# Kernel tuning notes

Measured on AMD Instinct MI355X. Metric: run time of the kernel, lower is better.

## Reference

```python
import jax, jax.numpy as jnp
import numpy as np

EMBED_DIM = 1024
LATEN_DIM = 1024
B, S = 4, 2048


def setup_inputs() -> dict:
    key = jax.random.key(0)
    k1, k2, k3, k4, k5 = jax.random.split(key, 5)
    xq = jax.random.normal(k1, (B, S, EMBED_DIM), dtype=jnp.float32)
    xk = jax.random.normal(k2, (B, S, EMBED_DIM), dtype=jnp.float32)
    xv = jax.random.normal(k3, (B, S, EMBED_DIM), dtype=jnp.float32)
    # Linear weight init similar to torch default scale
    bound = 1.0 / np.sqrt(EMBED_DIM)
    Wq = jax.random.uniform(k4, (EMBED_DIM, EMBED_DIM), minval=-bound, maxval=bound, dtype=jnp.float32)
    bq = jax.random.uniform(k5, (EMBED_DIM,), minval=-bound, maxval=bound, dtype=jnp.float32)
    # causal mask: 1 => masked (future positions)
    att_mask = jnp.triu(jnp.ones((S, S), dtype=jnp.int32), k=1)
    return {"xq": xq, "xk": xk, "xv": xv, "Wq": Wq, "bq": bq, "att_mask": att_mask}


def reference(xq, xk, xv, Wq, bq, att_mask):
    scale = LATEN_DIM ** (-0.5)
    # Faithful to source: linearQ is applied to all three inputs.
    Q = jnp.einsum('bsd,ed->bse', xq, Wq) + bq
    K = jnp.einsum('bsd,ed->bse', xk, Wq) + bq
    V = jnp.einsum('bsd,ed->bse', xv, Wq) + bq
    scores = jnp.einsum('bqe,bke->bqk', Q, K) * scale  # [B, S, S]
    scores = jnp.where(att_mask == 1, -jnp.inf, scores)
    probs = jax.nn.softmax(scores, axis=-1)
    return jnp.einsum('bqk,bke->bqe', probs, V)
```

## Files before the change

### kernel.cpp

```cpp
#include <hip/hip_runtime.h>
#include <hip/hip_bf16.h>
#include <stdint.h>


typedef __attribute__((ext_vector_type(8))) short bf16x8;
typedef __attribute__((ext_vector_type(4))) float floatx4;

#define DEVI static __device__ __forceinline__

static constexpr int S_ = 2048;
static constexpr int E_ = 1024;
static constexpr int BATCH = 4;

DEVI unsigned short f2b(float f) {
  union { float f; unsigned u; } v; v.f = f;
  return (unsigned short)((v.u + 0x7FFFu + ((v.u >> 16) & 1u)) >> 16);
}

DEVI void async_load16(const void* g, void* l) {
  __builtin_amdgcn_global_load_lds(
      (__attribute__((address_space(1))) void*)(void*)(g),
      (__attribute__((address_space(3))) void*)(l),
      16, 0, 0);
}

DEVI void mfma_tile(const unsigned short* lsA, const unsigned short* lsB,
                    int m0, int n0, int lrow, int lk, floatx4 (&acc)[4][4]) {
  bf16x8 af[4], bfr[4];
#pragma unroll
  for (int i = 0; i < 4; ++i)
    af[i] = *(const bf16x8*)(lsA + (m0 + i * 16 + lrow) * 32 + lk);
#pragma unroll
  for (int i = 0; i < 4; ++i)
    bfr[i] = *(const bf16x8*)(lsB + (n0 + i * 16 + lrow) * 32 + lk);
#pragma unroll
  for (int mi = 0; mi < 4; ++mi)
#pragma unroll
    for (int ni = 0; ni < 4; ++ni)
      acc[mi][ni] = __builtin_amdgcn_mfma_f32_16x16x32_bf16(
          af[mi], bfr[ni], acc[mi][ni], 0, 0, 0);
}

DEVI void stage_bf16(const unsigned short* src, unsigned short* ls, int ld,
                     int tid) {
#pragma unroll
  for (int j = 0; j < 2; ++j) {
    int t = tid + j * 256, row = t >> 2, kk = (t & 3) << 3;
    async_load16(src + (size_t)row * ld + kk, ls + t * 8);
  }
}

__global__ void cvt_kernel(const float* __restrict__ src,
                           unsigned short* __restrict__ dst, int n4) {
  int i = blockIdx.x * blockDim.x + threadIdx.x;
  if (i < n4) {
    float4 v = ((const float4*)src)[i];
    ushort4 o;
    o.x = f2b(v.x); o.y = f2b(v.y); o.z = f2b(v.z); o.w = f2b(v.w);
    ((ushort4*)dst)[i] = o;
  }
}

__global__ __launch_bounds__(256, 2) void gemm_qkv(
    const float* __restrict__ xq, const float* __restrict__ xk,
    const float* __restrict__ xv, const unsigned short* __restrict__ Wb,
    const float* __restrict__ bias, unsigned short* __restrict__ Qb,
    unsigned short* __restrict__ Kb, unsigned short* __restrict__ Vt) {
  __shared__ __align__(16) unsigned short lsA[128 * 32];
  __shared__ __align__(16) unsigned short lsB[128 * 32];
  const int l = blockIdx.x;
  const int xcd = l & 7, i = l >> 3;
  const int bn = i & 7;
  const int bmg = xcd * 24 + (i >> 3);
  const int input = bmg / 64, bm = bmg % 64;
  const float* A = (input == 0) ? xq : (input == 1) ? xk : xv;
  A += (size_t)bm * 128 * 1024;

  const int tid = threadIdx.x;
  const int lane = tid & 63, wave = tid >> 6;
  const int m0 = (wave >> 1) * 64, n0 = (wave & 1) * 64;
  const int lrow = lane & 15, lk = (lane >> 4) * 8;

  floatx4 acc[4][4] = {};

  for (int kt = 0; kt < 1024 / 32; ++kt) {
    if (kt) __syncthreads();
    stage_bf16(Wb + (size_t)bn * 128 * 1024 + kt * 32, lsB, 1024, tid);
#pragma unroll
    for (int j = 0; j < 4; ++j) {
      int t = tid + j * 256, row = t >> 3, kk = (t & 7) << 2;
      float4 v = *(const float4*)(A + (size_t)row * 1024 + kt * 32 + kk);
      ushort4 o;
      o.x = f2b(v.x); o.y = f2b(v.y); o.z = f2b(v.z); o.w = f2b(v.w);
      *(ushort4*)(lsA + row * 32 + kk) = o;
    }
    __syncthreads();
    mfma_tile(lsA, lsB, m0, n0, lrow, lk, acc);
  }

  unsigned short* C = (input == 0) ? Qb : (input == 1) ? Kb : Vt;
  const int rb = (lane >> 4) * 4;
#pragma unroll
  for (int mi = 0; mi < 4; ++mi)
#pragma unroll
    for (int ni = 0; ni < 4; ++ni) {
      int gcol = bn * 128 + n0 + ni * 16 + lrow;
      float bv = bias[gcol];
#pragma unroll
      for (int r = 0; r < 4; ++r) {
        int grow = bm * 128 + m0 + mi * 16 + rb + r;
        unsigned short val = f2b(acc[mi][ni][r] + bv);
        if (input == 2) {
          int b = grow >> 11, s = grow & 2047;
          C[((size_t)b * 1024 + gcol) * 2048 + s] = val;
        } else {
          C[(size_t)grow * 1024 + gcol] = val;
        }
      }
    }
}

__global__ __launch_bounds__(256, 2) void gemm_scores(
    const unsigned short* __restrict__ Qb,
    const unsigned short* __restrict__ Kb, float* __restrict__ Sc) {
  const int l = blockIdx.x;
  const int xcd = l & 7, k = l >> 3;
  const int m = k & 7, gl = k >> 3;
  const int gg = xcd * 12 + gl;
  const int z = gg / 24, r = gg % 24;
  const int bm = (r < 8) ? r : 8 + ((r - 8) >> 1);
  const int bn = ((r < 8) ? 0 : ((r - 8) & 1)) * 8 + m;
  if (bn > bm) return;

  __shared__ __align__(16) unsigned short lsA[128 * 32];
  __shared__ __align__(16) unsigned short lsB[128 * 32];
  const unsigned short* A = Qb + ((size_t)z * S_ + bm * 128) * E_;
  const unsigned short* Bt = Kb + ((size_t)z * S_ + bn * 128) * E_;
  float* C = Sc + (size_t)z * S_ * S_;
  const int tid = threadIdx.x;
  const int lane = tid & 63, wave = tid >> 6;
  const int m0 = (wave >> 1) * 64, n0 = (wave & 1) * 64;
  const int lrow = lane & 15, lk = (lane >> 4) * 8;

  floatx4 acc[4][4] = {};
  for (int kt = 0; kt < 32; ++kt) {
    if (kt) __syncthreads();
    stage_bf16(A + kt * 32, lsA, E_, tid);
    stage_bf16(Bt + kt * 32, lsB, E_, tid);
    __syncthreads();
    mfma_tile(lsA, lsB, m0, n0, lrow, lk, acc);
  }

  const int rb = (lane >> 4) * 4;
#pragma unroll
  for (int mi = 0; mi < 4; ++mi)
#pragma unroll
    for (int ni = 0; ni < 4; ++ni) {
      int gcol = bn * 128 + n0 + ni * 16 + lrow;
#pragma unroll
      for (int r = 0; r < 4; ++r) {
        int grow = bm * 128 + m0 + mi * 16 + rb + r;
        C[(size_t)grow * S_ + gcol] = acc[mi][ni][r] * 0.03125f;
      }
    }
}

__global__ __launch_bounds__(256, 2) void gemm_pv(
    const unsigned short* __restrict__ Pb,
    const unsigned short* __restrict__ Vt, float* __restrict__ Out) {
  __shared__ __align__(16) unsigned short lsA[128 * 32];
  __shared__ __align__(16) unsigned short lsB[128 * 32];
  const int l = blockIdx.x;
  const int xcd = l & 7, i = l >> 3;
  const int bn = i & 7;
  const int bmg = xcd * 8 + (i >> 3);
  const int z = bmg >> 4, bm = bmg & 15;

  const unsigned short* A = Pb + ((size_t)z * S_ + bm * 128) * (2 * S_);
  const unsigned short* Bt = Vt + ((size_t)z * E_ + bn * 128) * S_;
  float* C = Out + (size_t)z * S_ * E_;
  const int tid = threadIdx.x;
  const int lane = tid & 63, wave = tid >> 6;
  const int m0 = (wave >> 1) * 64, n0 = (wave & 1) * 64;
  const int lrow = lane & 15, lk = (lane >> 4) * 8;

  floatx4 acc[4][4] = {};
  const int nK = (bm + 1) * 4;
  for (int kt = 0; kt < nK; ++kt) {
    if (kt) __syncthreads();
    stage_bf16(A + kt * 32, lsA, 2 * S_, tid);
    stage_bf16(Bt + kt * 32, lsB, S_, tid);
    __syncthreads();
    mfma_tile(lsA, lsB, m0, n0, lrow, lk, acc);
  }

  const int rb = (lane >> 4) * 4;
#pragma unroll
  for (int mi = 0; mi < 4; ++mi)
#pragma unroll
    for (int ni = 0; ni < 4; ++ni) {
      int gcol = bn * 128 + n0 + ni * 16 + lrow;
#pragma unroll
      for (int r = 0; r < 4; ++r) {
        int grow = bm * 128 + m0 + mi * 16 + rb + r;
        C[(size_t)grow * E_ + gcol] = acc[mi][ni][r];
      }
    }
}

__global__ __launch_bounds__(256) void softmax_rows(float* __restrict__ Sc) {
  const int r = blockIdx.x;
  const int q = r & (S_ - 1);
  float* srow = Sc + (size_t)r * S_;
  __shared__ float buf[S_];
  __shared__ float red[8];
  const int tid = threadIdx.x, lane = tid & 63, wv = tid >> 6;
  const int n = q + 1;

  float mx = -1e30f;
  for (int k = tid; k < n; k += 256) {
    float v = srow[k];
    buf[k] = v;
    mx = fmaxf(mx, v);
  }
#pragma unroll
  for (int off = 32; off; off >>= 1) mx = fmaxf(mx, __shfl_xor(mx, off));
  if (lane == 0) red[wv] = mx;
  __syncthreads();
  mx = fmaxf(fmaxf(red[0], red[1]), fmaxf(red[2], red[3]));

  float sum = 0.f;
  for (int k = tid; k < n; k += 256) {
    float e = __expf(buf[k] - mx);
    buf[k] = e;
    sum += e;
  }
#pragma unroll
  for (int off = 32; off; off >>= 1) sum += __shfl_xor(sum, off);
  if (lane == 0) red[4 + wv] = sum;
  __syncthreads();
  sum = red[4] + red[5] + red[6] + red[7];
  const float inv = 1.0f / sum;

  unsigned short* prow = (unsigned short*)srow;
  const int kmax = (q & ~127) + 128;
  for (int k = tid; k < kmax; k += 256)
    prow[k] = (k < n) ? f2b(buf[k] * inv) : (unsigned short)0;
}

extern "C" void kernel_launch(void* const* d_in, const int* in_sizes, int n_in,
                              void* d_out, int out_size, void* d_ws,
                              size_t ws_size, hipStream_t stream) {
  (void)in_sizes; (void)n_in; (void)out_size; (void)ws_size;
  const float* xq = (const float*)d_in[0];
  const float* xk = (const float*)d_in[1];
  const float* xv = (const float*)d_in[2];
  const float* Wq = (const float*)d_in[3];
  const float* bq = (const float*)d_in[4];
  float* out = (float*)d_out;

  unsigned short* Wb = (unsigned short*)d_ws;
  unsigned short* Qb = Wb + (size_t)1024 * 1024;
  unsigned short* Kb = Qb + (size_t)8192 * 1024;
  unsigned short* Vt = Kb + (size_t)8192 * 1024;
  float* Sc = (float*)(Vt + (size_t)8192 * 1024);

  cvt_kernel<<<(1024 * 1024 / 4) / 256, 256, 0, stream>>>(Wq, Wb,
                                                          1024 * 1024 / 4);
  gemm_qkv<<<1536, 256, 0, stream>>>(xq, xk, xv, Wb, bq, Qb, Kb, Vt);
  gemm_scores<<<768, 256, 0, stream>>>(Qb, Kb, Sc);
  softmax_rows<<<BATCH * S_, 256, 0, stream>>>(Sc);
  gemm_pv<<<512, 256, 0, stream>>>((const unsigned short*)Sc, Vt, out);
}
```

Before: 341.0 us.

## Double-buffer LDS tiles in the QKV, scores and PV GEMM kernels

Measured after the change: 344.1 us. Within noise of the previous version (+0.9%).

```diff
diff --git a/kernel.cpp b/kernel.cpp
--- a/kernel.cpp
+++ b/kernel.cpp
@@ -66,8 +66,8 @@
     const float* __restrict__ xv, const unsigned short* __restrict__ Wb,
     const float* __restrict__ bias, unsigned short* __restrict__ Qb,
     unsigned short* __restrict__ Kb, unsigned short* __restrict__ Vt) {
-  __shared__ __align__(16) unsigned short lsA[128 * 32];
-  __shared__ __align__(16) unsigned short lsB[128 * 32];
+  __shared__ __align__(16) unsigned short lsA[2][128 * 32];
+  __shared__ __align__(16) unsigned short lsB[2][128 * 32];
   const int l = blockIdx.x;
   const int xcd = l & 7, i = l >> 3;
   const int bn = i & 7;
@@ -80,22 +80,46 @@
   const int lane = tid & 63, wave = tid >> 6;
   const int m0 = (wave >> 1) * 64, n0 = (wave & 1) * 64;
   const int lrow = lane & 15, lk = (lane >> 4) * 8;
+  const int ar0 = tid >> 3, ak0 = (tid & 7) << 2;
 
   floatx4 acc[4][4] = {};
 
-  for (int kt = 0; kt < 1024 / 32; ++kt) {
-    if (kt) __syncthreads();
-    stage_bf16(Wb + (size_t)bn * 128 * 1024 + kt * 32, lsB, 1024, tid);
+  stage_bf16(Wb + (size_t)bn * 128 * 1024, lsB[0], 1024, tid);
+  {
+    float4 v[4];
+#pragma unroll
+    for (int j = 0; j < 4; ++j)
+      v[j] = *(const float4*)(A + (size_t)(ar0 + j * 32) * 1024 + ak0);
 #pragma unroll
     for (int j = 0; j < 4; ++j) {
-      int t = tid + j * 256, row = t >> 3, kk = (t & 7) << 2;
-      float4 v = *(const float4*)(A + (size_t)row * 1024 + kt * 32 + kk);
       ushort4 o;
-      o.x = f2b(v.x); o.y = f2b(v.y); o.z = f2b(v.z); o.w = f2b(v.w);
-      *(ushort4*)(lsA + row * 32 + kk) = o;
-    }
+      o.x = f2b(v[j].x); o.y = f2b(v[j].y); o.z = f2b(v[j].z); o.w = f2b(v[j].w);
+      *(ushort4*)(lsA[0] + (ar0 + j * 32) * 32 + ak0) = o;
+    }
+  }
+
+  for (int kt = 0; kt < 32; ++kt) {
     __syncthreads();
-    mfma_tile(lsA, lsB, m0, n0, lrow, lk, acc);
+    const int cur = kt & 1, nxt = cur ^ 1;
+    float4 v[4];
+    if (kt < 31) {
+      stage_bf16(Wb + (size_t)bn * 128 * 1024 + (kt + 1) * 32, lsB[nxt], 1024,
+                 tid);
+#pragma unroll
+      for (int j = 0; j < 4; ++j)
+        v[j] = *(const float4*)(A + (size_t)(ar0 + j * 32) * 1024 +
+                                (kt + 1) * 32 + ak0);
+    }
+    mfma_tile(lsA[cur], lsB[cur], m0, n0, lrow, lk, acc);
+    if (kt < 31) {
+#pragma unroll
+      for (int j = 0; j < 4; ++j) {
+        ushort4 o;
+        o.x = f2b(v[j].x); o.y = f2b(v[j].y);
+        o.z = f2b(v[j].z); o.w = f2b(v[j].w);
+        *(ushort4*)(lsA[nxt] + (ar0 + j * 32) * 32 + ak0) = o;
+      }
+    }
   }
 
   unsigned short* C = (input == 0) ? Qb : (input == 1) ? Kb : Vt;
@@ -132,8 +156,8 @@
   const int bn = ((r < 8) ? 0 : ((r - 8) & 1)) * 8 + m;
   if (bn > bm) return;
 
-  __shared__ __align__(16) unsigned short lsA[128 * 32];
-  __shared__ __align__(16) unsigned short lsB[128 * 32];
+  __shared__ __align__(16) unsigned short lsA[2][128 * 32];
+  __shared__ __align__(16) unsigned short lsB[2][128 * 32];
   const unsigned short* A = Qb + ((size_t)z * S_ + bm * 128) * E_;
   const unsigned short* Bt = Kb + ((size_t)z * S_ + bn * 128) * E_;
   float* C = Sc + (size_t)z * S_ * S_;
@@ -143,12 +167,16 @@
   const int lrow = lane & 15, lk = (lane >> 4) * 8;
 
   floatx4 acc[4][4] = {};
+  stage_bf16(A, lsA[0], E_, tid);
+  stage_bf16(Bt, lsB[0], E_, tid);
   for (int kt = 0; kt < 32; ++kt) {
-    if (kt) __syncthreads();
-    stage_bf16(A + kt * 32, lsA, E_, tid);
-    stage_bf16(Bt + kt * 32, lsB, E_, tid);
     __syncthreads();
-    mfma_tile(lsA, lsB, m0, n0, lrow, lk, acc);
+    const int cur = kt & 1, nxt = cur ^ 1;
+    if (kt < 31) {
+      stage_bf16(A + (kt + 1) * 32, lsA[nxt], E_, tid);
+      stage_bf16(Bt + (kt + 1) * 32, lsB[nxt], E_, tid);
+    }
+    mfma_tile(lsA[cur], lsB[cur], m0, n0, lrow, lk, acc);
   }
 
   const int rb = (lane >> 4) * 4;
@@ -168,8 +196,8 @@
 __global__ __launch_bounds__(256, 2) void gemm_pv(
     const unsigned short* __restrict__ Pb,
     const unsigned short* __restrict__ Vt, float* __restrict__ Out) {
-  __shared__ __align__(16) unsigned short lsA[128 * 32];
-  __shared__ __align__(16) unsigned short lsB[128 * 32];
+  __shared__ __align__(16) unsigned short lsA[2][128 * 32];
+  __shared__ __align__(16) unsigned short lsB[2][128 * 32];
   const int l = blockIdx.x;
   const int xcd = l & 7, i = l >> 3;
   const int bn = i & 7;
@@ -186,12 +214,16 @@
 
   floatx4 acc[4][4] = {};
   const int nK = (bm + 1) * 4;
+  stage_bf16(A, lsA[0], 2 * S_, tid);
+  stage_bf16(Bt, lsB[0], S_, tid);
   for (int kt = 0; kt < nK; ++kt) {
-    if (kt) __syncthreads();
-    stage_bf16(A + kt * 32, lsA, 2 * S_, tid);
-    stage_bf16(Bt + kt * 32, lsB, S_, tid);
     __syncthreads();
-    mfma_tile(lsA, lsB, m0, n0, lrow, lk, acc);
+    const int cur = kt & 1, nxt = cur ^ 1;
+    if (kt < nK - 1) {
+      stage_bf16(A + (kt + 1) * 32, lsA[nxt], 2 * S_, tid);
+      stage_bf16(Bt + (kt + 1) * 32, lsB[nxt], S_, tid);
+    }
+    mfma_tile(lsA[cur], lsB[cur], m0, n0, lrow, lk, acc);
   }
 
   const int rb = (lane >> 4) * 4;
```

## Pre-convert activations to bf16 and double the K-step per barrier in GEMMs

Applied to the files above, without the earlier changes.

Measured after the change: 326.2 us. 1.05x faster.

```diff
diff --git a/kernel.cpp b/kernel.cpp
--- a/kernel.cpp
+++ b/kernel.cpp
@@ -61,20 +61,19 @@
   }
 }
 
-__global__ __launch_bounds__(256, 2) void gemm_qkv(
-    const float* __restrict__ xq, const float* __restrict__ xk,
-    const float* __restrict__ xv, const unsigned short* __restrict__ Wb,
+__global__ __launch_bounds__(256) void gemm_qkv(
+    const unsigned short* __restrict__ Xb, const unsigned short* __restrict__ Wb,
     const float* __restrict__ bias, unsigned short* __restrict__ Qb,
     unsigned short* __restrict__ Kb, unsigned short* __restrict__ Vt) {
-  __shared__ __align__(16) unsigned short lsA[128 * 32];
-  __shared__ __align__(16) unsigned short lsB[128 * 32];
+  __shared__ __align__(16) unsigned short lsA[2][128 * 32];
+  __shared__ __align__(16) unsigned short lsB[2][128 * 32];
   const int l = blockIdx.x;
   const int xcd = l & 7, i = l >> 3;
   const int bn = i & 7;
   const int bmg = xcd * 24 + (i >> 3);
   const int input = bmg / 64, bm = bmg % 64;
-  const float* A = (input == 0) ? xq : (input == 1) ? xk : xv;
-  A += (size_t)bm * 128 * 1024;
+  const unsigned short* A = Xb + (size_t)bmg * 128 * 1024;
+  const unsigned short* W = Wb + (size_t)bn * 128 * 1024;
 
   const int tid = threadIdx.x;
   const int lane = tid & 63, wave = tid >> 6;
@@ -83,19 +82,15 @@
 
   floatx4 acc[4][4] = {};
 
-  for (int kt = 0; kt < 1024 / 32; ++kt) {
+  for (int kt = 0; kt < 16; ++kt) {
     if (kt) __syncthreads();
-    stage_bf16(Wb + (size_t)bn * 128 * 1024 + kt * 32, lsB, 1024, tid);
-#pragma unroll
-    for (int j = 0; j < 4; ++j) {
-      int t = tid + j * 256, row = t >> 3, kk = (t & 7) << 2;
-      float4 v = *(const float4*)(A + (size_t)row * 1024 + kt * 32 + kk);
-      ushort4 o;
-      o.x = f2b(v.x); o.y = f2b(v.y); o.z = f2b(v.z); o.w = f2b(v.w);
-      *(ushort4*)(lsA + row * 32 + kk) = o;
-    }
+    stage_bf16(A + kt * 64, lsA[0], 1024, tid);
+    stage_bf16(A + kt * 64 + 32, lsA[1], 1024, tid);
+    stage_bf16(W + kt * 64, lsB[0], 1024, tid);
+    stage_bf16(W + kt * 64 + 32, lsB[1], 1024, tid);
     __syncthreads();
-    mfma_tile(lsA, lsB, m0, n0, lrow, lk, acc);
+    mfma_tile(lsA[0], lsB[0], m0, n0, lrow, lk, acc);
+    mfma_tile(lsA[1], lsB[1], m0, n0, lrow, lk, acc);
   }
 
   unsigned short* C = (input == 0) ? Qb : (input == 1) ? Kb : Vt;
@@ -120,7 +115,7 @@
     }
 }
 
-__global__ __launch_bounds__(256, 2) void gemm_scores(
+__global__ __launch_bounds__(256) void gemm_scores(
     const unsigned short* __restrict__ Qb,
     const unsigned short* __restrict__ Kb, float* __restrict__ Sc) {
   const int l = blockIdx.x;
@@ -132,8 +127,8 @@
   const int bn = ((r < 8) ? 0 : ((r - 8) & 1)) * 8 + m;
   if (bn > bm) return;
 
-  __shared__ __align__(16) unsigned short lsA[128 * 32];
-  __shared__ __align__(16) unsigned short lsB[128 * 32];
+  __shared__ __align__(16) unsigned short lsA[2][128 * 32];
+  __shared__ __align__(16) unsigned short lsB[2][128 * 32];
   const unsigned short* A = Qb + ((size_t)z * S_ + bm * 128) * E_;
   const unsigned short* Bt = Kb + ((size_t)z * S_ + bn * 128) * E_;
   float* C = Sc + (size_t)z * S_ * S_;
@@ -143,12 +138,15 @@
   const int lrow = lane & 15, lk = (lane >> 4) * 8;
 
   floatx4 acc[4][4] = {};
-  for (int kt = 0; kt < 32; ++kt) {
+  for (int kt = 0; kt < 16; ++kt) {
     if (kt) __syncthreads();
-    stage_bf16(A + kt * 32, lsA, E_, tid);
-    stage_bf16(Bt + kt * 32, lsB, E_, tid);
+    stage_bf16(A + kt * 64, lsA[0], E_, tid);
+    stage_bf16(A + kt * 64 + 32, lsA[1], E_, tid);
+    stage_bf16(Bt + kt * 64, lsB[0], E_, tid);
+    stage_bf16(Bt + kt * 64 + 32, lsB[1], E_, tid);
     __syncthreads();
-    mfma_tile(lsA, lsB, m0, n0, lrow, lk, acc);
+    mfma_tile(lsA[0], lsB[0], m0, n0, lrow, lk, acc);
+    mfma_tile(lsA[1], lsB[1], m0, n0, lrow, lk, acc);
   }
 
   const int rb = (lane >> 4) * 4;
@@ -165,11 +163,11 @@
     }
 }
 
-__global__ __launch_bounds__(256, 2) void gemm_pv(
+__global__ __launch_bounds__(256) void gemm_pv(
     const unsigned short* __restrict__ Pb,
     const unsigned short* __restrict__ Vt, float* __restrict__ Out) {
-  __shared__ __align__(16) unsigned short lsA[128 * 32];
-  __shared__ __align__(16) unsigned short lsB[128 * 32];
+  __shared__ __align__(16) unsigned short lsA[2][128 * 32];
+  __shared__ __align__(16) unsigned short lsB[2][128 * 32];
   const int l = blockIdx.x;
   const int xcd = l & 7, i = l >> 3;
   const int bn = i & 7;
@@ -185,13 +183,16 @@
   const int lrow = lane & 15, lk = (lane >> 4) * 8;
 
   floatx4 acc[4][4] = {};
-  const int nK = (bm + 1) * 4;
-  for (int kt = 0; kt < nK; ++kt) {
+  const int nKK = (bm + 1) * 2;
+  for (int kt = 0; kt < nKK; ++kt) {
     if (kt) __syncthreads();
-    stage_bf16(A + kt * 32, lsA, 2 * S_, tid);
-    stage_bf16(Bt + kt * 32, lsB, S_, tid);
+    stage_bf16(A + kt * 64, lsA[0], 2 * S_, tid);
+    stage_bf16(A + kt * 64 + 32, lsA[1], 2 * S_, tid);
+    stage_bf16(Bt + kt * 64, lsB[0], S_, tid);
+    stage_bf16(Bt + kt * 64 + 32, lsB[1], S_, tid);
     __syncthreads();
-    mfma_tile(lsA, lsB, m0, n0, lrow, lk, acc);
+    mfma_tile(lsA[0], lsB[0], m0, n0, lrow, lk, acc);
+    mfma_tile(lsA[1], lsB[1], m0, n0, lrow, lk, acc);
   }
 
   const int rb = (lane >> 4) * 4;
@@ -259,15 +260,23 @@
   const float* bq = (const float*)d_in[4];
   float* out = (float*)d_out;
 
-  unsigned short* Wb = (unsigned short*)d_ws;
+  unsigned short* base16 = (unsigned short*)d_ws;
+  unsigned short* Xb = base16;
+  float* Sc = (float*)d_ws;
+  unsigned short* Wb = base16 + (size_t)32 * 1024 * 1024;
   unsigned short* Qb = Wb + (size_t)1024 * 1024;
   unsigned short* Kb = Qb + (size_t)8192 * 1024;
   unsigned short* Vt = Kb + (size_t)8192 * 1024;
-  float* Sc = (float*)(Vt + (size_t)8192 * 1024);
-
+
+  const int n4x = 8192 * 1024 / 4;
+  cvt_kernel<<<n4x / 256, 256, 0, stream>>>(xq, Xb, n4x);
+  cvt_kernel<<<n4x / 256, 256, 0, stream>>>(xk, Xb + (size_t)8192 * 1024, n4x);
+  cvt_kernel<<<n4x / 256, 256, 0, stream>>>(xv, Xb + (size_t)2 * 8192 * 1024,
+                                            n4x);
   cvt_kernel<<<(1024 * 1024 / 4) / 256, 256, 0, stream>>>(Wq, Wb,
                                                           1024 * 1024 / 4);
-  gemm_qkv<<<1536, 256, 0, stream>>>(xq, xk, xv, Wb, bq, Qb, Kb, Vt);
+
+  gemm_qkv<<<1536, 256, 0, stream>>>(Xb, Wb, bq, Qb, Kb, Vt);
   gemm_scores<<<768, 256, 0, stream>>>(Qb, Kb, Sc);
   softmax_rows<<<BATCH * S_, 256, 0, stream>>>(Sc);
   gemm_pv<<<512, 256, 0, stream>>>((const unsigned short*)Sc, Vt, out);
```
